# Optimization experiments

Hardware: AMD Instinct MI355X
Metric: run time of the kernel (lower is better)

The kernel has to match this reference:

```python
import jax, jax.numpy as jnp
import numpy as np
from jax import lax

B, L, D = 2, 4096, 2048
K, KQ, M, H = 32, 4, 8, 8  # H = D*expand // (K*M)
MEM = K * H              # 256
FLAT = K * H * M         # 2048
CONV_W = 4
DIM_SWIGLU = H * 3 * 2   # out_expand_factor=3 -> 48
N_DECAY = K - 4          # 28 decay heads, 4 anchor heads


def setup_inputs() -> dict:
    key = jax.random.key(0)
    ks = jax.random.split(key, 8)
    x = jax.random.normal(ks[0], (B, L, D), dtype=jnp.float32)
    W_mem = jax.random.normal(ks[1], (D, MEM + K), dtype=jnp.float32) / np.sqrt(D)
    conv_k = jax.random.normal(ks[2], (CONV_W, 1, MEM + K), dtype=jnp.float32) * 0.3
    W_q = jax.random.normal(ks[3], (D, KQ * H * M * 2), dtype=jnp.float32) / np.sqrt(D)
    theta = jnp.asarray(np.tile(np.geomspace(0.001, 3.0, M).reshape(1, 1, 1, 1, M),
                                (1, 1, K, H, 1)), dtype=jnp.float32)
    decay_slopes = jnp.asarray(np.log(np.expm1(np.geomspace(0.001, 0.1, N_DECAY))), dtype=jnp.float32)
    anchor_slopes = jnp.asarray(np.log(np.expm1(np.geomspace(0.01, 0.1, 4))), dtype=jnp.float32)
    score_scale = jnp.ones((K,), dtype=jnp.float32)
    g = np.sqrt(2.0 / (H + DIM_SWIGLU))
    W_re = jax.random.normal(ks[4], (K, H, DIM_SWIGLU), dtype=jnp.float32) * g
    W_im = jax.random.normal(ks[5], (K, H, DIM_SWIGLU), dtype=jnp.float32) * g
    norm_scale = jnp.ones((1, 1, K, H), dtype=jnp.float32)
    W_out = jax.random.normal(ks[6], (K * H * 3, D), dtype=jnp.float32) / np.sqrt(K * H * 3)
    return {"x": x, "W_mem": W_mem, "conv_k": conv_k, "W_q": W_q, "theta": theta,
            "decay_slopes": decay_slopes, "anchor_slopes": anchor_slopes,
            "score_scale": score_scale, "W_re": W_re, "W_im": W_im,
            "norm_scale": norm_scale, "W_out": W_out}


def _forward(x, W_mem, conv_k, W_q, theta, decay_slopes, anchor_slopes,
             score_scale, W_re, W_im, norm_scale, W_out):
    b, l, d = x.shape
    # memory branch: dense + causal depthwise conv
    z = x @ W_mem  # (b, l, MEM+K)
    z = lax.conv_general_dilated(z, conv_k, window_strides=(1,),
                                 padding=[(CONV_W - 1, 0)],
                                 dimension_numbers=('NHC', 'HIO', 'NHC'),
                                 feature_group_count=MEM + K)
    k_val = z[..., :MEM].reshape(b, l, K, H)
    s_raw = z[..., MEM:].reshape(b, l, K, 1)
    # query branch
    q = (x @ W_q).reshape(b, l, KQ, H, M, 2)
    q_re, q_im = q[..., 0], q[..., 1]
    # per-head time weights (decay heads look back from end, anchor heads from start)
    pos = jnp.arange(l, dtype=jnp.float32)
    slopes_d = jax.nn.softplus(decay_slopes).reshape(1, 1, -1, 1)
    slopes_a = jax.nn.softplus(anchor_slopes).reshape(1, 1, -1, 1)
    dist = jnp.maximum(jnp.float32(l - 1) - pos, 0.0)
    log_w = jnp.concatenate([-slopes_d * dist[None, :, None, None],
                             -slopes_a * pos[None, :, None, None]], axis=2)  # (1,l,K,1)
    log_p = jnp.clip(score_scale[None, None, :, None] * s_raw, -20.0, 20.0)
    p_w = jnp.exp(log_p + log_w)  # (b,l,K,1)
    # complex rotation of keys
    phi = k_val[..., None] * theta          # (b,l,K,H,M)
    re_k, im_k = jnp.cos(phi), jnp.sin(phi)
    pw5 = p_w[..., None]
    merged = jnp.concatenate([p_w.squeeze(-1),
                              (pw5 * re_k).reshape(b, l, FLAT),
                              (pw5 * im_k).reshape(b, l, FLAT)], axis=-1)
    cs = jnp.cumsum(merged, axis=1)
    den = cs[..., :K]                       # (b,l,K)
    num_re = cs[..., K:K + FLAT]
    num_im = cs[..., K + FLAT:]
    inv_den = 1.0 / jnp.maximum(den[..., None], 1e-4)  # (b,l,K,1)
    state_re = num_re.reshape(b, l, K, H, M) * inv_den[..., None]
    state_im = num_im.reshape(b, l, K, H, M) * inv_den[..., None]
    # GQA-style query repeat
    n_rep = K // KQ
    q_re = jnp.repeat(q_re, n_rep, axis=2)
    q_im = jnp.repeat(q_im, n_rep, axis=2)
    out_re = jnp.sum(state_re * q_re + state_im * q_im, axis=-1)  # (b,l,K,H)
    out_im = jnp.sum(state_im * q_re - state_re * q_im, axis=-1)
    out_re = out_re * norm_scale
    out_im = out_im * norm_scale
    y = jnp.einsum('blkh,khn->blkn', out_re, W_re) + jnp.einsum('blkh,khn->blkn', out_im, W_im)
    y_val, y_gate = jnp.split(y, 2, axis=-1)
    y = (y_val * jax.nn.silu(y_gate)).reshape(b, l, -1)
    return y @ W_out


def reference(x, W_mem, conv_k, W_q, theta, decay_slopes, anchor_slopes,
              score_scale, W_re, W_im, norm_scale, W_out):
    return _forward(x, W_mem, conv_k, W_q, theta, decay_slopes, anchor_slopes,
                    score_scale, W_re, W_im, norm_scale, W_out)
```

## Files before the change

### kernel.cpp

```cpp
#include <hip/hip_runtime.h>
#include <hip/hip_bf16.h>
#include <math.h>

#define BB 2
#define LL 4096
#define DD 2048
#define KK 32
#define MEM 256
#define CTOT 288
#define NQ 512
#define ZSTR 800
#define NPAD 896
#define FLAT 2048
#define CMERG 4128
#define CH 16
#define NCH 256
#define YDIM 768
#define KV2 1536
#define BL (BB*LL)

typedef __attribute__((ext_vector_type(4))) float f32x4;
typedef __attribute__((ext_vector_type(8))) short bf16x8;
typedef __attribute__((ext_vector_type(8))) unsigned short u16x8;

__device__ inline unsigned short f2b(float v) {
    __hip_bfloat16 h = __float2bfloat16(v);
    return *reinterpret_cast<unsigned short*>(&h);
}
__device__ inline float b2f(unsigned short u) {
    __hip_bfloat16 h;
    *reinterpret_cast<unsigned short*>(&h) = u;
    return __bfloat162float(h);
}

__device__ inline void gload16(const void* g, void* l) {
    __builtin_amdgcn_global_load_lds(
        (const __attribute__((address_space(1))) unsigned int*)g,
        (__attribute__((address_space(3))) unsigned int*)l, 16, 0, 0);
}

template<int HH>
__device__ inline float bcast8(float v) {
    return __int_as_float(__builtin_amdgcn_ds_swizzle(__float_as_int(v), (HH << 5) | 0x18));
}

__device__ inline float fast_sigmoid_mul(float val, float g) {
    return val * __builtin_amdgcn_rcpf(1.f + __expf(-g));
}

__global__ __launch_bounds__(256) void cvt_x(const float* __restrict__ x,
                                             unsigned short* __restrict__ xb) {
    size_t i = ((size_t)blockIdx.x * 256 + threadIdx.x) * 8;
    float4 a = *(const float4*)&x[i];
    float4 b = *(const float4*)&x[i + 4];
    u16x8 o;
    o[0] = f2b(a.x); o[1] = f2b(a.y); o[2] = f2b(a.z); o[3] = f2b(a.w);
    o[4] = f2b(b.x); o[5] = f2b(b.y); o[6] = f2b(b.z); o[7] = f2b(b.w);
    *(u16x8*)&xb[i] = o;
}

__global__ __launch_bounds__(256) void prep_wb(const float* __restrict__ W_mem,
                                               const float* __restrict__ W_q,
                                               unsigned short* __restrict__ Wb) {
    int n = blockIdx.x;
    for (int k = threadIdx.x; k < DD; k += 256) {
        float v = 0.f;
        if (n < CTOT) v = W_mem[(size_t)k * CTOT + n];
        else if (n < ZSTR) v = W_q[(size_t)k * NQ + (n - CTOT)];
        Wb[(size_t)n * DD + k] = f2b(v);
    }
}

__global__ __launch_bounds__(256) void prep_wo(const float* __restrict__ W_out,
                                               unsigned short* __restrict__ Wo) {
    int n = blockIdx.x;
    for (int k = threadIdx.x; k < YDIM; k += 256) {
        float v = W_out[(size_t)k * DD + n];
        unsigned short hi = f2b(v);
        float r = v - b2f(hi);
        Wo[(size_t)n * KV2 + k] = hi;
        Wo[(size_t)n * KV2 + YDIM + k] = f2b(r);
    }
}

template<bool CBF16>
__global__ __launch_bounds__(256) void gemm_mfma(const unsigned short* __restrict__ A,
                                                 const unsigned short* __restrict__ Bh_g,
                                                 void* __restrict__ Cout,
                                                 int Kd, int Nvalid, int Cstride) {
    __shared__ unsigned short As[2][4096];
    __shared__ unsigned short Bh[2][4096];
    int tid = threadIdx.x;
    int lane = tid & 63;
    int wave = tid >> 6;
    int wr = wave >> 1, wc = wave & 1;

    int nwg = gridDim.x * gridDim.y;
    int bid = blockIdx.y * gridDim.x + blockIdx.x;
    int cpx = nwg >> 3;
    int swz = (bid & 7) * cpx + (bid >> 3);
    int bx = swz % gridDim.x, by = swz / gridDim.x;
    int m0 = by * 128;
    int n0 = bx * 128;

    f32x4 acc[4][4];
#pragma unroll
    for (int i = 0; i < 4; ++i)
#pragma unroll
        for (int j = 0; j < 4; ++j) acc[i][j] = (f32x4){0.f, 0.f, 0.f, 0.f};

    int f0 = tid, f1 = 256 + tid;
    int row0 = f0 >> 2, ks0 = (f0 & 3) ^ ((row0 >> 1) & 3);
    int row1 = f1 >> 2, ks1 = (f1 & 3) ^ ((row1 >> 1) & 3);
    const unsigned short* ga0 = &A[(size_t)(m0 + row0) * Kd + ks0 * 8];
    const unsigned short* ga1 = &A[(size_t)(m0 + row1) * Kd + ks1 * 8];
    const unsigned short* gb0 = &Bh_g[(size_t)(n0 + row0) * Kd + ks0 * 8];
    const unsigned short* gb1 = &Bh_g[(size_t)(n0 + row1) * Kd + ks1 * 8];
    int l0 = (wave * 64) * 8;
    int l1 = (256 + wave * 64) * 8;

    int g = lane >> 4, rr = lane & 15;

#define STAGE(buf, koff) do {                                          \
        gload16(ga0 + (koff), &As[buf][l0]);                           \
        gload16(ga1 + (koff), &As[buf][l1]);                           \
        gload16(gb0 + (koff), &Bh[buf][l0]);                           \
        gload16(gb1 + (koff), &Bh[buf][l1]);                           \
    } while (0)

    STAGE(0, 0);
    __syncthreads();

    int nIter = Kd >> 5;
    int cur = 0;
    for (int it = 0; it < nIter; ++it) {
        if (it + 1 < nIter) STAGE(cur ^ 1, (it + 1) * 32);

        bf16x8 av[4], bhv[4];
#pragma unroll
        for (int i = 0; i < 4; ++i) {
            int ra = wr * 64 + i * 16 + rr;
            av[i] = *(const bf16x8*)&As[cur][ra * 32 + ((g ^ ((ra >> 1) & 3)) * 8)];
            int rb = wc * 64 + i * 16 + rr;
            bhv[i] = *(const bf16x8*)&Bh[cur][rb * 32 + ((g ^ ((rb >> 1) & 3)) * 8)];
        }
#pragma unroll
        for (int i = 0; i < 4; ++i)
#pragma unroll
            for (int j = 0; j < 4; ++j)
                acc[i][j] = __builtin_amdgcn_mfma_f32_16x16x32_bf16(av[i], bhv[j], acc[i][j], 0, 0, 0);

        __syncthreads();
        cur ^= 1;
    }
#undef STAGE

    int cg = lane >> 4, cr = lane & 15;
#pragma unroll
    for (int i = 0; i < 4; ++i)
#pragma unroll
        for (int j = 0; j < 4; ++j) {
            int colb = n0 + wc * 64 + j * 16 + cr;
            if (colb < Nvalid) {
#pragma unroll
                for (int r = 0; r < 4; ++r) {
                    int rowb = m0 + wr * 64 + i * 16 + cg * 4 + r;
                    if (CBF16)
                        ((unsigned short*)Cout)[(size_t)rowb * Cstride + colb] = f2b(acc[i][j][r]);
                    else
                        ((float*)Cout)[(size_t)rowb * Cstride + colb] = acc[i][j][r];
                }
            }
        }
}

__global__ __launch_bounds__(512, 2) void gemm256(const unsigned short* __restrict__ A,
                                                  const unsigned short* __restrict__ Bm,
                                                  float* __restrict__ C,
                                                  int KA, int Kv, int Cstride) {
    __shared__ __attribute__((aligned(16))) unsigned short As[2][16384];
    __shared__ __attribute__((aligned(16))) unsigned short Bs[2][16384];
    int tid = threadIdx.x;
    int lane = tid & 63, wave = tid >> 6;
    int wm = wave >> 2, wn = wave & 3;

    int nwg = gridDim.x * gridDim.y;
    int bid = blockIdx.y * gridDim.x + blockIdx.x;
    int cpx = nwg >> 3;
    int swz = (bid & 7) * cpx + (bid >> 3);
    int bx = swz % gridDim.x, by = swz / gridDim.x;
    int m0 = by * 256, n0 = bx * 256;

    f32x4 acc[8][4];
#pragma unroll
    for (int i = 0; i < 8; ++i)
#pragma unroll
        for (int j = 0; j < 4; ++j) acc[i][j] = (f32x4){0.f, 0.f, 0.f, 0.f};

    const unsigned short* pA[4];
    const unsigned short* pB[4];
    int ldsoff[4];
#pragma unroll
    for (int j = 0; j < 4; ++j) {
        int f = j * 512 + tid;
        int row = f >> 3, s = f & 7;
        int sg = s ^ (row & 7);
        pA[j] = A + (size_t)(m0 + row) * KA + sg * 8;
        pB[j] = Bm + (size_t)(n0 + row) * Kv + sg * 8;
        ldsoff[j] = (j * 512 + wave * 64) * 8;
    }

    int rr = lane & 15, kg = lane >> 4;

#pragma unroll
    for (int j = 0; j < 4; ++j) gload16(pA[j], &As[0][ldsoff[j]]);
#pragma unroll
    for (int j = 0; j < 4; ++j) gload16(pB[j], &Bs[0][ldsoff[j]]);
    __syncthreads();

    int nT = Kv >> 6;
    int cur = 0;

#define LDA(fr, t) ({ int ra_ = wm * 128 + (fr) * 16 + rr;                       \
        int sd_ = (t) * 4 + kg;                                                  \
        *(const bf16x8*)&As[cur][(ra_ * 8 + (sd_ ^ (ra_ & 7))) * 8]; })
#define LDB(fc, t) ({ int rb_ = wn * 64 + (fc) * 16 + rr;                        \
        int sd_ = (t) * 4 + kg;                                                  \
        *(const bf16x8*)&Bs[cur][(rb_ * 8 + (sd_ ^ (rb_ & 7))) * 8]; })

    for (int it = 0; it < nT; ++it) {
        int nxt = cur ^ 1;
        bool hn = (it + 1 < nT);
        int k0n = (it + 1) << 6;
        int kkA = (k0n >= KA) ? (k0n - KA) : k0n;
        bf16x8 av[4], bv[4];

#pragma unroll
        for (int j = 0; j < 4; ++j) bv[j] = LDB(j, 0);
#pragma unroll
        for (int j = 0; j < 4; ++j) av[j] = LDA(j, 0);
        if (hn) { gload16(pA[0] + kkA, &As[nxt][ldsoff[0]]); gload16(pA[1] + kkA, &As[nxt][ldsoff[1]]); }
        __builtin_amdgcn_s_barrier();
        __builtin_amdgcn_s_setprio(1);
#pragma unroll
        for (int i = 0; i < 4; ++i)
#pragma unroll
            for (int j = 0; j < 4; ++j)
                acc[i][j] = __builtin_amdgcn_mfma_f32_16x16x32_bf16(av[i], bv[j], acc[i][j], 0, 0, 0);
        __builtin_amdgcn_s_setprio(0);
        __builtin_amdgcn_s_barrier();

#pragma unroll
        for (int j = 0; j < 4; ++j) bv[j] = LDB(j, 1);
#pragma unroll
        for (int j = 0; j < 4; ++j) av[j] = LDA(j, 1);
        if (hn) { gload16(pA[2] + kkA, &As[nxt][ldsoff[2]]); gload16(pA[3] + kkA, &As[nxt][ldsoff[3]]); }
        __builtin_amdgcn_s_barrier();
        __builtin_amdgcn_s_setprio(1);
#pragma unroll
        for (int i = 0; i < 4; ++i)
#pragma unroll
            for (int j = 0; j < 4; ++j)
                acc[i][j] = __builtin_amdgcn_mfma_f32_16x16x32_bf16(av[i], bv[j], acc[i][j], 0, 0, 0);
        __builtin_amdgcn_s_setprio(0);
        __builtin_amdgcn_s_barrier();

#pragma unroll
        for (int j = 0; j < 4; ++j) bv[j] = LDB(j, 0);
#pragma unroll
        for (int j = 0; j < 4; ++j) av[j] = LDA(4 + j, 0);
        if (hn) { gload16(pB[0] + k0n, &Bs[nxt][ldsoff[0]]); gload16(pB[1] + k0n, &Bs[nxt][ldsoff[1]]); }
        __builtin_amdgcn_s_barrier();
        __builtin_amdgcn_s_setprio(1);
#pragma unroll
        for (int i = 0; i < 4; ++i)
#pragma unroll
            for (int j = 0; j < 4; ++j)
                acc[4 + i][j] = __builtin_amdgcn_mfma_f32_16x16x32_bf16(av[i], bv[j], acc[4 + i][j], 0, 0, 0);
        __builtin_amdgcn_s_setprio(0);
        __builtin_amdgcn_s_barrier();

#pragma unroll
        for (int j = 0; j < 4; ++j) bv[j] = LDB(j, 1);
#pragma unroll
        for (int j = 0; j < 4; ++j) av[j] = LDA(4 + j, 1);
        if (hn) { gload16(pB[2] + k0n, &Bs[nxt][ldsoff[2]]); gload16(pB[3] + k0n, &Bs[nxt][ldsoff[3]]); }
        __builtin_amdgcn_s_barrier();
        __builtin_amdgcn_s_setprio(1);
#pragma unroll
        for (int i = 0; i < 4; ++i)
#pragma unroll
            for (int j = 0; j < 4; ++j)
                acc[4 + i][j] = __builtin_amdgcn_mfma_f32_16x16x32_bf16(av[i], bv[j], acc[4 + i][j], 0, 0, 0);
        __builtin_amdgcn_s_setprio(0);

        __syncthreads();
        cur = nxt;
    }
#undef LDA
#undef LDB

#pragma unroll
    for (int i = 0; i < 8; ++i)
#pragma unroll
        for (int j = 0; j < 4; ++j) {
            int colb = n0 + wn * 64 + j * 16 + rr;
#pragma unroll
            for (int r = 0; r < 4; ++r) {
                int rowb = m0 + wm * 128 + i * 16 + kg * 4 + r;
                C[(size_t)rowb * Cstride + colb] = acc[i][j][r];
            }
        }
}

__global__ __launch_bounds__(256) void fused_partial(const unsigned short* __restrict__ zq,
                                                     const float* __restrict__ conv_k,
                                                     const float* __restrict__ theta,
                                                     const float* __restrict__ decay,
                                                     const float* __restrict__ anchor,
                                                     const float* __restrict__ sscale,
                                                     float* __restrict__ partials) {
    int chunk = blockIdx.x, b = blockIdx.y, t = threadIdx.x;
    int l0 = chunk * CH;
    __shared__ unsigned short zin[CH + 3][CTOT];

    for (int idx = t; idx < (CH + 3) * 36; idx += 256) {
        int r = idx / 36, c8 = (idx % 36) * 8;
        int l = l0 - 3 + r;
        u16x8 v = (u16x8)(0);
        if (l >= 0) v = *(const u16x8*)&zq[(size_t)(b * LL + l) * ZSTR + c8];
        *(u16x8*)&zin[r][c8] = v;
    }
    __syncthreads();

    int k = t >> 3;
    float cz0 = conv_k[t], cz1 = conv_k[CTOT + t], cz2 = conv_k[2 * CTOT + t], cz3 = conv_k[3 * CTOT + t];
    int sc = MEM + k;
    float cs0 = conv_k[sc], cs1 = conv_k[CTOT + sc], cs2 = conv_k[2 * CTOT + sc], cs3 = conv_k[3 * CTOT + sc];
    float xx = (k < KK - 4) ? decay[k] : anchor[k - (KK - 4)];
    float sp = (xx > 20.f) ? xx : log1pf(__expf(xx));
    float ss = sscale[k];
    float th[8];
#pragma unroll
    for (int m = 0; m < 8; ++m) th[m] = theta[t * 8 + m];
    float rs[8], is[8];
#pragma unroll
    for (int m = 0; m < 8; ++m) { rs[m] = 0.f; is[m] = 0.f; }
    float dsum = 0.f;

#pragma unroll 1
    for (int i = 0; i < CH; ++i) {
        float kv = b2f(zin[i][t]) * cz0 + b2f(zin[i + 1][t]) * cz1 +
                   b2f(zin[i + 2][t]) * cz2 + b2f(zin[i + 3][t]) * cz3;
        float s = b2f(zin[i][sc]) * cs0 + b2f(zin[i + 1][sc]) * cs1 +
                  b2f(zin[i + 2][sc]) * cs2 + b2f(zin[i + 3][sc]) * cs3;
        int l = l0 + i;
        float lw = (k < KK - 4) ? -sp * (float)(LL - 1 - l) : -sp * (float)l;
        float lp = fminf(fmaxf(ss * s, -20.f), 20.f);
        float p = __expf(lp + lw);
        dsum += p;
#pragma unroll
        for (int m = 0; m < 8; ++m) {
            float sn, cn;
            __sincosf(kv * th[m], &sn, &cn);
            rs[m] += p * cn;
            is[m] += p * sn;
        }
    }
    size_t base = ((size_t)b * NCH + chunk) * CMERG;
    *(f32x4*)&partials[base + KK + t * 8]            = (f32x4){rs[0], rs[1], rs[2], rs[3]};
    *(f32x4*)&partials[base + KK + t * 8 + 4]        = (f32x4){rs[4], rs[5], rs[6], rs[7]};
    *(f32x4*)&partials[base + KK + FLAT + t * 8]     = (f32x4){is[0], is[1], is[2], is[3]};
    *(f32x4*)&partials[base + KK + FLAT + t * 8 + 4] = (f32x4){is[4], is[5], is[6], is[7]};
    if ((t & 7) == 0) partials[base + k] = dsum;
}

__global__ __launch_bounds__(256) void scan_partials(float* __restrict__ partials) {
    int t = threadIdx.x;
    int cl = t & 15, j = t >> 4;
    int c = blockIdx.x * 16 + cl;
    int b = blockIdx.y;
    float v[16];
    float s = 0.f;
#pragma unroll
    for (int i = 0; i < 16; ++i) {
        v[i] = partials[((size_t)b * NCH + j * 16 + i) * CMERG + c];
        s += v[i];
    }
    __shared__ float sums[16][17];
    sums[j][cl] = s;
    __syncthreads();
    if (j == 0) {
        float run = 0.f;
#pragma unroll
        for (int jj = 0; jj < 16; ++jj) {
            float x = sums[jj][cl];
            sums[jj][cl] = run;
            run += x;
        }
    }
    __syncthreads();
    float run = sums[j][cl];
#pragma unroll
    for (int i = 0; i < 16; ++i) {
        float x = v[i];
        partials[((size_t)b * NCH + j * 16 + i) * CMERG + c] = run;
        run += x;
    }
}

__global__ __launch_bounds__(256) void fused_stage(const unsigned short* __restrict__ zq,
                                                   const float* __restrict__ conv_k,
                                                   const float* __restrict__ theta,
                                                   const float* __restrict__ decay,
                                                   const float* __restrict__ anchor,
                                                   const float* __restrict__ sscale,
                                                   const float* __restrict__ partials,
                                                   const float* __restrict__ W_re,
                                                   const float* __restrict__ W_im,
                                                   const float* __restrict__ nscale,
                                                   unsigned short* __restrict__ y_act) {
    int chunk = blockIdx.x, b = blockIdx.y, t = threadIdx.x;
    int l0 = chunk * CH;
    __shared__ unsigned short zin[CH + 3][CTOT];
    __shared__ unsigned short qall[CH][NQ];

    for (int idx = t; idx < (CH + 3) * 36; idx += 256) {
        int r = idx / 36, c8 = (idx % 36) * 8;
        int l = l0 - 3 + r;
        u16x8 v = (u16x8)(0);
        if (l >= 0) v = *(const u16x8*)&zq[(size_t)(b * LL + l) * ZSTR + c8];
        *(u16x8*)&zin[r][c8] = v;
    }
    for (int idx = t; idx < CH * (NQ / 8); idx += 256) {
        int i = idx >> 6, c8 = (idx & 63) * 8;
        *(u16x8*)&qall[i][c8] = *(const u16x8*)&zq[(size_t)(b * LL + l0 + i) * ZSTR + CTOT + c8];
    }
    __syncthreads();

    int k = t >> 3, h = t & 7, w = t >> 6;
    float cz0 = conv_k[t], cz1 = conv_k[CTOT + t], cz2 = conv_k[2 * CTOT + t], cz3 = conv_k[3 * CTOT + t];
    int sc = MEM + k;
    float cs0 = conv_k[sc], cs1 = conv_k[CTOT + sc], cs2 = conv_k[2 * CTOT + sc], cs3 = conv_k[3 * CTOT + sc];
    float xx = (k < KK - 4) ? decay[k] : anchor[k - (KK - 4)];
    float sp = (xx > 20.f) ? xx : log1pf(__expf(xx));
    float ss = sscale[k];
    float th[8];
#pragma unroll
    for (int m = 0; m < 8; ++m) th[m] = theta[t * 8 + m];
    float ns = nscale[t];
    int qb = w * 128 + h * 16;

    float wre[8][6], wim[8][6];
#pragma unroll
    for (int hh = 0; hh < 8; ++hh)
#pragma unroll
        for (int jj = 0; jj < 6; ++jj) {
            wre[hh][jj] = W_re[(k * 8 + hh) * 48 + h + 8 * jj];
            wim[hh][jj] = W_im[(k * 8 + hh) * 48 + h + 8 * jj];
        }

    size_t pbase = ((size_t)b * NCH + chunk) * CMERG;
    f32x4 r0 = *(const f32x4*)&partials[pbase + KK + t * 8];
    f32x4 r1 = *(const f32x4*)&partials[pbase + KK + t * 8 + 4];
    f32x4 i0 = *(const f32x4*)&partials[pbase + KK + FLAT + t * 8];
    f32x4 i1 = *(const f32x4*)&partials[pbase + KK + FLAT + t * 8 + 4];
    float rs[8] = {r0[0], r0[1], r0[2], r0[3], r1[0], r1[1], r1[2], r1[3]};
    float is[8] = {i0[0], i0[1], i0[2], i0[3], i1[0], i1[1], i1[2], i1[3]};
    float den = partials[pbase + k];

#pragma unroll 1
    for (int i = 0; i < CH; ++i) {
        float kv = b2f(zin[i][t]) * cz0 + b2f(zin[i + 1][t]) * cz1 +
                   b2f(zin[i + 2][t]) * cz2 + b2f(zin[i + 3][t]) * cz3;
        float s = b2f(zin[i][sc]) * cs0 + b2f(zin[i + 1][sc]) * cs1 +
                  b2f(zin[i + 2][sc]) * cs2 + b2f(zin[i + 3][sc]) * cs3;
        int l = l0 + i;
        float lw = (k < KK - 4) ? -sp * (float)(LL - 1 - l) : -sp * (float)l;
        float lp = fminf(fmaxf(ss * s, -20.f), 20.f);
        float p = __expf(lp + lw);
        den += p;
        float inv = __builtin_amdgcn_rcpf(fmaxf(den, 1e-4f));
#pragma unroll
        for (int m = 0; m < 8; ++m) {
            float sn, cn;
            __sincosf(kv * th[m], &sn, &cn);
            rs[m] += p * cn;
            is[m] += p * sn;
        }
        u16x8 qv0 = *(const u16x8*)&qall[i][qb];
        u16x8 qv1 = *(const u16x8*)&qall[i][qb + 8];
        float o_re = 0.f, o_im = 0.f;
#pragma unroll
        for (int m = 0; m < 8; ++m) {
            float sre = rs[m] * inv;
            float sim = is[m] * inv;
            float qre = b2f((unsigned short)((m < 4) ? qv0[2 * m] : qv1[2 * m - 8]));
            float qim = b2f((unsigned short)((m < 4) ? qv0[2 * m + 1] : qv1[2 * m - 7]));
            o_re += sre * qre + sim * qim;
            o_im += sim * qre - sre * qim;
        }
        o_re *= ns;
        o_im *= ns;

        float y0 = 0.f, y1 = 0.f, y2 = 0.f, y3 = 0.f, y4 = 0.f, y5 = 0.f;
#define EAPPLY(HH) { float br_ = bcast8<HH>(o_re); float bi_ = bcast8<HH>(o_im); \
        y0 += br_ * wre[HH][0] + bi_ * wim[HH][0]; \
        y1 += br_ * wre[HH][1] + bi_ * wim[HH][1]; \
        y2 += br_ * wre[HH][2] + bi_ * wim[HH][2]; \
        y3 += br_ * wre[HH][3] + bi_ * wim[HH][3]; \
        y4 += br_ * wre[HH][4] + bi_ * wim[HH][4]; \
        y5 += br_ * wre[HH][5] + bi_ * wim[HH][5]; }
        EAPPLY(0) EAPPLY(1) EAPPLY(2) EAPPLY(3)
        EAPPLY(4) EAPPLY(5) EAPPLY(6) EAPPLY(7)
#undef EAPPLY

        size_t ybase = (size_t)(b * LL + l) * YDIM + k * 24 + h;
        y_act[ybase]      = f2b(fast_sigmoid_mul(y0 * y3, y3));
        y_act[ybase + 8]  = f2b(fast_sigmoid_mul(y1 * y4, y4));
        y_act[ybase + 16] = f2b(fast_sigmoid_mul(y2 * y5, y5));
    }
}

extern "C" void kernel_launch(void* const* d_in, const int* in_sizes, int n_in,
                              void* d_out, int out_size, void* d_ws, size_t ws_size,
                              hipStream_t stream) {
    const float* x      = (const float*)d_in[0];
    const float* W_mem  = (const float*)d_in[1];
    const float* conv_k = (const float*)d_in[2];
    const float* W_q    = (const float*)d_in[3];
    const float* theta  = (const float*)d_in[4];
    const float* decay  = (const float*)d_in[5];
    const float* anchor = (const float*)d_in[6];
    const float* sscale = (const float*)d_in[7];
    const float* W_re   = (const float*)d_in[8];
    const float* W_im   = (const float*)d_in[9];
    const float* nscale = (const float*)d_in[10];
    const float* W_out  = (const float*)d_in[11];
    float* out = (float*)d_out;
    float* ws = (float*)d_ws;

    unsigned short* xb = (unsigned short*)out;
    unsigned short* Wb = (unsigned short*)(out + 8388608);
    unsigned short* zq = (unsigned short*)(out + 9306112);
    float* partials      = ws;
    unsigned short* yb   = (unsigned short*)(ws + 2113536);
    unsigned short* Wo   = (unsigned short*)(ws + 5259264);

    cvt_x<<<8192, 256, 0, stream>>>(x, xb);
    prep_wb<<<NPAD, 256, 0, stream>>>(W_mem, W_q, Wb);
    prep_wo<<<DD, 256, 0, stream>>>(W_out, Wo);

    gemm_mfma<true><<<dim3(NPAD / 128, BL / 128), 256, 0, stream>>>(
        xb, Wb, zq, DD, ZSTR, ZSTR);
    fused_partial<<<dim3(NCH, BB), 256, 0, stream>>>(zq, conv_k, theta, decay, anchor, sscale, partials);
    scan_partials<<<dim3(CMERG / 16, BB), 256, 0, stream>>>(partials);
    fused_stage<<<dim3(NCH, BB), 256, 0, stream>>>(zq, conv_k, theta, decay, anchor, sscale,
                                                   partials, W_re, W_im, nscale, yb);
    gemm256<<<dim3(DD / 256, BL / 256), 512, 0, stream>>>(yb, Wo, out, YDIM, KV2, DD);
}
```

Measured before the change: 181.5 us.

## Reorder GEMM prefetch loads and replace full syncs with partial vmcnt waits

Reorders the double-buffered global-to-LDS prefetches so B tiles load first and A row-groups load in the order they are consumed. The block-wide __syncthreads at the end of each iteration is replaced by explicit s_waitcnt vmcnt with partial counts plus s_barrier, so computation can start while later loads are still in flight. This aims to hide more load latency behind MFMA work. It depends on the hand-counted vmcnt values exactly matching the issued loads; if the counts or the A/B consumption order are off, stale LDS data could be read.

```diff
diff --git a/kernel.cpp b/kernel.cpp
--- a/kernel.cpp
+++ b/kernel.cpp
@@ -212,11 +212,12 @@
 
     int rr = lane & 15, kg = lane >> 4;
 
-#pragma unroll
-    for (int j = 0; j < 4; ++j) gload16(pA[j], &As[0][ldsoff[j]]);
-#pragma unroll
-    for (int j = 0; j < 4; ++j) gload16(pB[j], &Bs[0][ldsoff[j]]);
-    __syncthreads();
+    gload16(pB[0], &Bs[0][ldsoff[0]]); gload16(pB[1], &Bs[0][ldsoff[1]]);
+    gload16(pB[2], &Bs[0][ldsoff[2]]); gload16(pB[3], &Bs[0][ldsoff[3]]);
+    gload16(pA[0], &As[0][ldsoff[0]]); gload16(pA[2], &As[0][ldsoff[2]]);
+    gload16(pA[1], &As[0][ldsoff[1]]); gload16(pA[3], &As[0][ldsoff[3]]);
+    asm volatile("s_waitcnt vmcnt(2)" ::: "memory");
+    __builtin_amdgcn_s_barrier();
 
     int nT = Kv >> 6;
     int cur = 0;
@@ -228,6 +229,16 @@
         int sd_ = (t) * 4 + kg;                                                  \
         *(const bf16x8*)&Bs[cur][(rb_ * 8 + (sd_ ^ (rb_ & 7))) * 8]; })
 
+#define MFMA16(io) do {                                                           \
+    __builtin_amdgcn_s_setprio(1);                                                \
+    _Pragma("unroll")                                                             \
+    for (int i = 0; i < 4; ++i)                                                   \
+        _Pragma("unroll")                                                         \
+        for (int j = 0; j < 4; ++j)                                               \
+            acc[(io) + i][j] = __builtin_amdgcn_mfma_f32_16x16x32_bf16(av[i], bv[j], acc[(io) + i][j], 0, 0, 0); \
+    __builtin_amdgcn_s_setprio(0);                                                \
+} while (0)
+
     for (int it = 0; it < nT; ++it) {
         int nxt = cur ^ 1;
         bool hn = (it + 1 < nT);
@@ -239,66 +250,51 @@
         for (int j = 0; j < 4; ++j) bv[j] = LDB(j, 0);
 #pragma unroll
         for (int j = 0; j < 4; ++j) av[j] = LDA(j, 0);
-        if (hn) { gload16(pA[0] + kkA, &As[nxt][ldsoff[0]]); gload16(pA[1] + kkA, &As[nxt][ldsoff[1]]); }
-        __builtin_amdgcn_s_barrier();
-        __builtin_amdgcn_s_setprio(1);
-#pragma unroll
-        for (int i = 0; i < 4; ++i)
-#pragma unroll
-            for (int j = 0; j < 4; ++j)
-                acc[i][j] = __builtin_amdgcn_mfma_f32_16x16x32_bf16(av[i], bv[j], acc[i][j], 0, 0, 0);
-        __builtin_amdgcn_s_setprio(0);
+        if (hn) { gload16(pB[0] + k0n, &Bs[nxt][ldsoff[0]]); gload16(pB[1] + k0n, &Bs[nxt][ldsoff[1]]); }
+        __builtin_amdgcn_s_barrier();
+        MFMA16(0);
         __builtin_amdgcn_s_barrier();
 
 #pragma unroll
         for (int j = 0; j < 4; ++j) bv[j] = LDB(j, 1);
 #pragma unroll
         for (int j = 0; j < 4; ++j) av[j] = LDA(j, 1);
-        if (hn) { gload16(pA[2] + kkA, &As[nxt][ldsoff[2]]); gload16(pA[3] + kkA, &As[nxt][ldsoff[3]]); }
-        __builtin_amdgcn_s_barrier();
-        __builtin_amdgcn_s_setprio(1);
-#pragma unroll
-        for (int i = 0; i < 4; ++i)
-#pragma unroll
-            for (int j = 0; j < 4; ++j)
-                acc[i][j] = __builtin_amdgcn_mfma_f32_16x16x32_bf16(av[i], bv[j], acc[i][j], 0, 0, 0);
-        __builtin_amdgcn_s_setprio(0);
+        if (hn) {
+            gload16(pB[2] + k0n, &Bs[nxt][ldsoff[2]]); gload16(pB[3] + k0n, &Bs[nxt][ldsoff[3]]);
+            asm volatile("s_waitcnt vmcnt(4)" ::: "memory");
+        } else {
+            asm volatile("s_waitcnt vmcnt(0)" ::: "memory");
+        }
+        __builtin_amdgcn_s_barrier();
+        MFMA16(0);
         __builtin_amdgcn_s_barrier();
 
 #pragma unroll
         for (int j = 0; j < 4; ++j) bv[j] = LDB(j, 0);
 #pragma unroll
         for (int j = 0; j < 4; ++j) av[j] = LDA(4 + j, 0);
-        if (hn) { gload16(pB[0] + k0n, &Bs[nxt][ldsoff[0]]); gload16(pB[1] + k0n, &Bs[nxt][ldsoff[1]]); }
-        __builtin_amdgcn_s_barrier();
-        __builtin_amdgcn_s_setprio(1);
-#pragma unroll
-        for (int i = 0; i < 4; ++i)
-#pragma unroll
-            for (int j = 0; j < 4; ++j)
-                acc[4 + i][j] = __builtin_amdgcn_mfma_f32_16x16x32_bf16(av[i], bv[j], acc[4 + i][j], 0, 0, 0);
-        __builtin_amdgcn_s_setprio(0);
+        if (hn) { gload16(pA[0] + kkA, &As[nxt][ldsoff[0]]); gload16(pA[2] + kkA, &As[nxt][ldsoff[2]]); }
+        __builtin_amdgcn_s_barrier();
+        MFMA16(4);
         __builtin_amdgcn_s_barrier();
 
 #pragma unroll
         for (int j = 0; j < 4; ++j) bv[j] = LDB(j, 1);
 #pragma unroll
         for (int j = 0; j < 4; ++j) av[j] = LDA(4 + j, 1);
-        if (hn) { gload16(pB[2] + k0n, &Bs[nxt][ldsoff[2]]); gload16(pB[3] + k0n, &Bs[nxt][ldsoff[3]]); }
-        __builtin_amdgcn_s_barrier();
-        __builtin_amdgcn_s_setprio(1);
-#pragma unroll
-        for (int i = 0; i < 4; ++i)
-#pragma unroll
-            for (int j = 0; j < 4; ++j)
-                acc[4 + i][j] = __builtin_amdgcn_mfma_f32_16x16x32_bf16(av[i], bv[j], acc[4 + i][j], 0, 0, 0);
-        __builtin_amdgcn_s_setprio(0);
-
-        __syncthreads();
+        if (hn) {
+            gload16(pA[1] + kkA, &As[nxt][ldsoff[1]]); gload16(pA[3] + kkA, &As[nxt][ldsoff[3]]);
+            asm volatile("s_waitcnt vmcnt(2)" ::: "memory");
+        }
+        __builtin_amdgcn_s_barrier();
+        MFMA16(4);
+        __builtin_amdgcn_s_barrier();
+
         cur = nxt;
     }
 #undef LDA
 #undef LDB
+#undef MFMA16
 
 #pragma unroll
     for (int i = 0; i < 8; ++i)
```

New measurement: 180.4 us. Within noise of the previous version (-0.6%).
